# Kernel tuning notes

Measured on AMD Instinct MI355X. Metric: run time of the kernel, lower is better.

The kernel has to match this reference:

```python
import jax, jax.numpy as jnp
import numpy as np

NUM_CODES = 512
DIM = 64
B, M = 32, 64


def setup_inputs() -> dict:
    key = jax.random.key(0)
    k1, k2 = jax.random.split(key)
    inputs = jax.random.normal(k1, (B, M, M, DIM), dtype=jnp.float32)
    # keras 'uniform' initializer is U(-0.05, 0.05)
    embeddings = jax.random.uniform(k2, (NUM_CODES, DIM), dtype=jnp.float32,
                                    minval=-0.05, maxval=0.05)
    return {"inputs": inputs, "embeddings": embeddings}


def reference(inputs, embeddings):
    l2_inputs = jnp.sum(inputs * inputs, axis=-1, keepdims=True)      # [B,M,M,1]
    l2_embeddings = jnp.sum(embeddings * embeddings, axis=-1)          # [K]
    dot = jnp.einsum('bhwd,kd->bhwk', inputs, embeddings)              # [B,M,M,K]
    distance = l2_inputs + l2_embeddings - 2.0 * dot                   # [B,M,M,K]
    codes = jnp.argmin(distance, axis=-1).astype(jnp.int32)            # [B,M,M]
    code_vecs = embeddings[codes]                                      # [B,M,M,D]
    return codes, code_vecs
```

## Files before the change

kernel.cpp:

```cpp
#include <hip/hip_runtime.h>

#define NUM_CODES 512
#define DIM 64
#define NPIX (32 * 64 * 64)
#define CT (NUM_CODES / 16)
#define BLK 256
#define NGRP 2
#define PPB 128

typedef __attribute__((ext_vector_type(8))) short bf16x8;
typedef __attribute__((ext_vector_type(4))) float f32x4;

__device__ __forceinline__ unsigned short f2bf(float f) {
    unsigned u = __float_as_uint(f);
    return (unsigned short)((u + 0x7fffu + ((u >> 16) & 1u)) >> 16);
}
__device__ __forceinline__ float bf2f(unsigned short h) {
    return __uint_as_float(((unsigned)h) << 16);
}

__global__ __launch_bounds__(256) void prep_kernel(
    const float* __restrict__ emb, unsigned short* __restrict__ AH,
    unsigned short* __restrict__ ALO, float* __restrict__ l2e,
    float* __restrict__ l2eh) {
    const int t = blockIdx.x * 256 + threadIdx.x;
    const int e0 = t * 4;
    const int c = e0 >> 6, d0 = e0 & 63;
    const float4 v = *(const float4*)(emb + c * DIM + d0);
    float f[4] = {-v.x, -v.y, -v.z, -v.w};
    unsigned short h[4], l[4];
#pragma unroll
    for (int i = 0; i < 4; ++i) {
        h[i] = f2bf(f[i]);
        l[i] = f2bf(f[i] - bf2f(h[i]));
    }
    const int ct = c >> 4, mr = c & 15, s = d0 >> 5, q = (d0 & 31) >> 3,
              j0 = d0 & 7;
    const int base = ((ct * 2 + s) * 64 + (q * 16 + mr)) * 8 + j0;
    *(ushort4*)(AH + base) = make_ushort4(h[0], h[1], h[2], h[3]);
    *(ushort4*)(ALO + base) = make_ushort4(l[0], l[1], l[2], l[3]);

    if (t < NUM_CODES) {
        const float* e = emb + t * DIM;
        float r[8];
#pragma unroll
        for (int j = 0; j < 8; ++j) {
            float w = e[j];
            r[j] = w * w;
        }
#pragma unroll
        for (int i = 8; i < DIM; i += 8)
#pragma unroll
            for (int j = 0; j < 8; ++j) {
                float w = e[i + j];
                r[j] += w * w;
            }
        float sv =
            ((r[0] + r[1]) + (r[2] + r[3])) + ((r[4] + r[5]) + (r[6] + r[7]));
        l2e[t] = sv;
        l2eh[t] = 0.5f * sv;
    }
}

__global__ __launch_bounds__(BLK, 4) void vq_main(
    const float* __restrict__ x_in, const unsigned short* __restrict__ AH,
    const unsigned short* __restrict__ ALO, const float* __restrict__ l2e,
    const float* __restrict__ l2eh, const float* __restrict__ emb,
    float* __restrict__ codes_out, float* __restrict__ vecs_out) {
    __shared__ float s_l2eh[NUM_CODES];
    __shared__ float s_l2ex[NUM_CODES];
    __shared__ int s_top[PPB][2];
    __shared__ int s_code[PPB];

    const int tid = threadIdx.x, lane = tid & 63, wave = tid >> 6;
    s_l2eh[tid] = l2eh[tid];
    s_l2eh[tid + 256] = l2eh[tid + 256];
    s_l2ex[tid] = l2e[tid];
    s_l2ex[tid + 256] = l2e[tid + 256];
    __syncthreads();

    const int p = lane & 15, q = lane >> 4;
    const int pw = blockIdx.x * PPB + wave * (16 * NGRP);

    bf16x8 bh0[NGRP], bl0[NGRP], bh1[NGRP], bl1[NGRP];
#pragma unroll
    for (int g = 0; g < NGRP; ++g) {
        const float* xb = x_in + (size_t)(pw + g * 16 + p) * DIM + q * 8;
        float4 u0 = *(const float4*)(xb);
        float4 u1 = *(const float4*)(xb + 4);
        float4 u2 = *(const float4*)(xb + 32);
        float4 u3 = *(const float4*)(xb + 36);
        float f0[8] = {u0.x, u0.y, u0.z, u0.w, u1.x, u1.y, u1.z, u1.w};
        float f1[8] = {u2.x, u2.y, u2.z, u2.w, u3.x, u3.y, u3.z, u3.w};
#pragma unroll
        for (int j = 0; j < 8; ++j) {
            unsigned short hh = f2bf(f0[j]);
            bh0[g][j] = (short)hh;
            bl0[g][j] = (short)f2bf(f0[j] - bf2f(hh));
            unsigned short h2 = f2bf(f1[j]);
            bh1[g][j] = (short)h2;
            bl1[g][j] = (short)f2bf(f1[j] - bf2f(h2));
        }
    }

    const int rowbase = q * 4;
    float d1[NGRP], d2[NGRP];
    int k1[NGRP], k2[NGRP];
#pragma unroll
    for (int g = 0; g < NGRP; ++g) {
        d1[g] = 3.4e38f;
        d2[g] = 3.4e38f;
        k1[g] = 0;
        k2[g] = 0;
    }

    const unsigned short* pAH = AH + lane * 8;
    const unsigned short* pAL = ALO + lane * 8;

    bf16x8 a0h = *(const bf16x8*)(pAH);
    bf16x8 a0l = *(const bf16x8*)(pAL);
    bf16x8 a1h = *(const bf16x8*)(pAH + 512);
    bf16x8 a1l = *(const bf16x8*)(pAL + 512);

    for (int ct = 0; ct < CT; ++ct) {
        const int nt = (ct + 1) & (CT - 1);
        const bf16x8 n0h = *(const bf16x8*)(pAH + nt * 1024);
        const bf16x8 n0l = *(const bf16x8*)(pAL + nt * 1024);
        const bf16x8 n1h = *(const bf16x8*)(pAH + nt * 1024 + 512);
        const bf16x8 n1l = *(const bf16x8*)(pAL + nt * 1024 + 512);

        const int kb = ct * 16 + rowbase;
        const f32x4 acc_init = *(const f32x4*)&s_l2eh[kb];

#pragma unroll
        for (int g = 0; g < NGRP; ++g) {
            f32x4 acc = acc_init;
            acc = __builtin_amdgcn_mfma_f32_16x16x32_bf16(a0h, bh0[g], acc, 0, 0, 0);
            acc = __builtin_amdgcn_mfma_f32_16x16x32_bf16(a1h, bh1[g], acc, 0, 0, 0);
            acc = __builtin_amdgcn_mfma_f32_16x16x32_bf16(a0l, bh0[g], acc, 0, 0, 0);
            acc = __builtin_amdgcn_mfma_f32_16x16x32_bf16(a1l, bh1[g], acc, 0, 0, 0);
            acc = __builtin_amdgcn_mfma_f32_16x16x32_bf16(a0h, bl0[g], acc, 0, 0, 0);
            acc = __builtin_amdgcn_mfma_f32_16x16x32_bf16(a1h, bl1[g], acc, 0, 0, 0);

#pragma unroll
            for (int r = 0; r < 4; ++r) {
                const float d = acc[r];
                const int kk = kb + r;
                const bool c = d < d1[g], c2 = d < d2[g];
                const float nd2 = __builtin_amdgcn_fmed3f(d1[g], d2[g], d);
                const int nk2 = c2 ? kk : k2[g];
                k2[g] = c ? k1[g] : nk2;
                k1[g] = c ? kk : k1[g];
                d2[g] = nd2;
                d1[g] = fminf(d1[g], d);
            }
        }
        a0h = n0h;
        a0l = n0l;
        a1h = n1h;
        a1l = n1l;
    }

#pragma unroll
    for (int g = 0; g < NGRP; ++g) {
        float a1 = d1[g], a2 = d2[g];
        int b1 = k1[g], b2 = k2[g];
#pragma unroll
        for (int off = 16; off <= 32; off <<= 1) {
            const float od1 = __shfl_xor(a1, off);
            const int ok1 = __shfl_xor(b1, off);
            const float od2 = __shfl_xor(a2, off);
            const int ok2 = __shfl_xor(b2, off);
            const bool c = od1 < a1;
            const float w1 = c ? od1 : a1;
            const int wk1 = c ? ok1 : b1;
            const float l1 = c ? a1 : od1;
            const int lk1 = c ? b1 : ok1;
            const bool cm = od2 < a2;
            const float m2 = cm ? od2 : a2;
            const int mk2 = cm ? ok2 : b2;
            const bool c3 = m2 < l1;
            a2 = c3 ? m2 : l1;
            b2 = c3 ? mk2 : lk1;
            a1 = w1;
            b1 = wk1;
        }
        if (lane < 16) {
            const int pb = wave * (16 * NGRP) + g * 16 + lane;
            s_top[pb][0] = b1;
            s_top[pb][1] = b2;
        }
    }
    __syncthreads();

    if (tid < PPB) {
        const int pix = blockIdx.x * PPB + tid;
        int ka = s_top[tid][0], kb2 = s_top[tid][1];
        if (kb2 < ka) {
            const int tt = ka;
            ka = kb2;
            kb2 = tt;
        }
        const float* xr = x_in + (size_t)pix * DIM;
        float x[DIM];
#pragma unroll
        for (int jj = 0; jj < 16; ++jj) {
            const float4 v = *(const float4*)(xr + jj * 4);
            x[4 * jj + 0] = v.x;
            x[4 * jj + 1] = v.y;
            x[4 * jj + 2] = v.z;
            x[4 * jj + 3] = v.w;
        }
        float r[8];
#pragma unroll
        for (int j = 0; j < 8; ++j) r[j] = x[j] * x[j];
#pragma unroll
        for (int i = 8; i < DIM; i += 8)
#pragma unroll
            for (int j = 0; j < 8; ++j) r[j] += x[i + j] * x[i + j];
        const float l2x =
            ((r[0] + r[1]) + (r[2] + r[3])) + ((r[4] + r[5]) + (r[6] + r[7]));

        const float* ea = emb + (size_t)ka * DIM;
        float acca = 0.f;
#pragma unroll
        for (int d = 0; d < DIM; ++d) acca = __builtin_fmaf(x[d], ea[d], acca);
        const float da = (l2x + s_l2ex[ka]) - 2.0f * acca;

        const float* eb = emb + (size_t)kb2 * DIM;
        float accb = 0.f;
#pragma unroll
        for (int d = 0; d < DIM; ++d) accb = __builtin_fmaf(x[d], eb[d], accb);
        const float db = (l2x + s_l2ex[kb2]) - 2.0f * accb;

        const int sel = (db < da) ? kb2 : ka;
        s_code[tid] = sel;
        codes_out[pix] = (float)sel;
    }
    __syncthreads();

    const float4* emb4 = (const float4*)emb;
    float4* vout4 = (float4*)(vecs_out + (size_t)blockIdx.x * PPB * DIM);
#pragma unroll
    for (int it = 0; it < (PPB * DIM / 4) / BLK; ++it) {
        const int fidx = tid + it * BLK;
        const int pp = fidx >> 4, dd = fidx & 15;
        vout4[fidx] = emb4[(size_t)s_code[pp] * (DIM / 4) + dd];
    }
}

extern "C" void kernel_launch(void* const* d_in, const int* in_sizes, int n_in,
                              void* d_out, int out_size, void* d_ws,
                              size_t ws_size, hipStream_t stream) {
    const float* x_in = (const float*)d_in[0];
    const float* emb = (const float*)d_in[1];

    unsigned short* AH = (unsigned short*)d_ws;
    unsigned short* ALO = AH + NUM_CODES * DIM;
    float* l2e = (float*)(ALO + NUM_CODES * DIM);
    float* l2eh = l2e + NUM_CODES;

    float* codes_out = (float*)d_out;
    float* vecs_out = (float*)d_out + NPIX;

    hipLaunchKernelGGL(prep_kernel, dim3(32), dim3(256), 0, stream, emb, AH,
                       ALO, l2e, l2eh);
    hipLaunchKernelGGL(vq_main, dim3(NPIX / PPB), dim3(BLK), 0, stream, x_in,
                       AH, ALO, l2e, l2eh, emb, codes_out, vecs_out);
}
```

Measured before the change: 126.2 us.

## Deepen codebook prefetch, split MFMA chains, and parallelize top-2 refinement across all threads

The codebook tile loads are now issued two tiles ahead instead of one, and the loop is unrolled by four to hide global-load latency. Each group's six dependent MFMAs are split into two independent accumulator chains of three and summed afterwards, which shortens the dependency chain. The MFMA block is wrapped in s_setprio. The exact fp32 re-check of the two candidates now runs on all 256 threads, one candidate per thread, with a shuffle to pick the winner, instead of 128 threads each doing two dot products. This costs more registers and each x row is loaded twice.

```diff
diff --git a/kernel.cpp b/kernel.cpp
--- a/kernel.cpp
+++ b/kernel.cpp
@@ -117,34 +117,48 @@
     const unsigned short* pAH = AH + lane * 8;
     const unsigned short* pAL = ALO + lane * 8;
 
-    bf16x8 a0h = *(const bf16x8*)(pAH);
-    bf16x8 a0l = *(const bf16x8*)(pAL);
-    bf16x8 a1h = *(const bf16x8*)(pAH + 512);
-    bf16x8 a1l = *(const bf16x8*)(pAL + 512);
-
+    bf16x8 c0h = *(const bf16x8*)(pAH);
+    bf16x8 c0l = *(const bf16x8*)(pAL);
+    bf16x8 c1h = *(const bf16x8*)(pAH + 512);
+    bf16x8 c1l = *(const bf16x8*)(pAL + 512);
+    bf16x8 p0h = *(const bf16x8*)(pAH + 1024);
+    bf16x8 p0l = *(const bf16x8*)(pAL + 1024);
+    bf16x8 p1h = *(const bf16x8*)(pAH + 1024 + 512);
+    bf16x8 p1l = *(const bf16x8*)(pAL + 1024 + 512);
+
+#pragma unroll 4
     for (int ct = 0; ct < CT; ++ct) {
-        const int nt = (ct + 1) & (CT - 1);
-        const bf16x8 n0h = *(const bf16x8*)(pAH + nt * 1024);
-        const bf16x8 n0l = *(const bf16x8*)(pAL + nt * 1024);
-        const bf16x8 n1h = *(const bf16x8*)(pAH + nt * 1024 + 512);
-        const bf16x8 n1l = *(const bf16x8*)(pAL + nt * 1024 + 512);
+        const int nt = (ct + 2) & (CT - 1);
+        const bf16x8 q0h = *(const bf16x8*)(pAH + nt * 1024);
+        const bf16x8 q0l = *(const bf16x8*)(pAL + nt * 1024);
+        const bf16x8 q1h = *(const bf16x8*)(pAH + nt * 1024 + 512);
+        const bf16x8 q1l = *(const bf16x8*)(pAL + nt * 1024 + 512);
 
         const int kb = ct * 16 + rowbase;
         const f32x4 acc_init = *(const f32x4*)&s_l2eh[kb];
 
+        f32x4 accA[NGRP], accB[NGRP];
+        __builtin_amdgcn_s_setprio(1);
 #pragma unroll
         for (int g = 0; g < NGRP; ++g) {
-            f32x4 acc = acc_init;
-            acc = __builtin_amdgcn_mfma_f32_16x16x32_bf16(a0h, bh0[g], acc, 0, 0, 0);
-            acc = __builtin_amdgcn_mfma_f32_16x16x32_bf16(a1h, bh1[g], acc, 0, 0, 0);
-            acc = __builtin_amdgcn_mfma_f32_16x16x32_bf16(a0l, bh0[g], acc, 0, 0, 0);
-            acc = __builtin_amdgcn_mfma_f32_16x16x32_bf16(a1l, bh1[g], acc, 0, 0, 0);
-            acc = __builtin_amdgcn_mfma_f32_16x16x32_bf16(a0h, bl0[g], acc, 0, 0, 0);
-            acc = __builtin_amdgcn_mfma_f32_16x16x32_bf16(a1h, bl1[g], acc, 0, 0, 0);
-
+            f32x4 a = acc_init;
+            a = __builtin_amdgcn_mfma_f32_16x16x32_bf16(c0h, bh0[g], a, 0, 0, 0);
+            a = __builtin_amdgcn_mfma_f32_16x16x32_bf16(c0l, bh0[g], a, 0, 0, 0);
+            a = __builtin_amdgcn_mfma_f32_16x16x32_bf16(c0h, bl0[g], a, 0, 0, 0);
+            f32x4 b = {0.f, 0.f, 0.f, 0.f};
+            b = __builtin_amdgcn_mfma_f32_16x16x32_bf16(c1h, bh1[g], b, 0, 0, 0);
+            b = __builtin_amdgcn_mfma_f32_16x16x32_bf16(c1l, bh1[g], b, 0, 0, 0);
+            b = __builtin_amdgcn_mfma_f32_16x16x32_bf16(c1h, bl1[g], b, 0, 0, 0);
+            accA[g] = a;
+            accB[g] = b;
+        }
+        __builtin_amdgcn_s_setprio(0);
+
+#pragma unroll
+        for (int g = 0; g < NGRP; ++g) {
 #pragma unroll
             for (int r = 0; r < 4; ++r) {
-                const float d = acc[r];
+                const float d = accA[g][r] + accB[g][r];
                 const int kk = kb + r;
                 const bool c = d < d1[g], c2 = d < d2[g];
                 const float nd2 = __builtin_amdgcn_fmed3f(d1[g], d2[g], d);
@@ -155,10 +169,9 @@
                 d1[g] = fminf(d1[g], d);
             }
         }
-        a0h = n0h;
-        a0l = n0l;
-        a1h = n1h;
-        a1l = n1l;
+
+        c0h = p0h; c0l = p0l; c1h = p1h; c1l = p1l;
+        p0h = q0h; p0l = q0l; p1h = q1h; p1l = q1l;
     }
 
 #pragma unroll
@@ -193,14 +206,10 @@
     }
     __syncthreads();
 
-    if (tid < PPB) {
-        const int pix = blockIdx.x * PPB + tid;
-        int ka = s_top[tid][0], kb2 = s_top[tid][1];
-        if (kb2 < ka) {
-            const int tt = ka;
-            ka = kb2;
-            kb2 = tt;
-        }
+    {
+        const int pixloc = tid >> 1, which = tid & 1;
+        const int pix = blockIdx.x * PPB + pixloc;
+        const int k_me = s_top[pixloc][which];
         const float* xr = x_in + (size_t)pix * DIM;
         float x[DIM];
 #pragma unroll
@@ -221,21 +230,20 @@
         const float l2x =
             ((r[0] + r[1]) + (r[2] + r[3])) + ((r[4] + r[5]) + (r[6] + r[7]));
 
-        const float* ea = emb + (size_t)ka * DIM;
-        float acca = 0.f;
-#pragma unroll
-        for (int d = 0; d < DIM; ++d) acca = __builtin_fmaf(x[d], ea[d], acca);
-        const float da = (l2x + s_l2ex[ka]) - 2.0f * acca;
-
-        const float* eb = emb + (size_t)kb2 * DIM;
-        float accb = 0.f;
-#pragma unroll
-        for (int d = 0; d < DIM; ++d) accb = __builtin_fmaf(x[d], eb[d], accb);
-        const float db = (l2x + s_l2ex[kb2]) - 2.0f * accb;
-
-        const int sel = (db < da) ? kb2 : ka;
-        s_code[tid] = sel;
-        codes_out[pix] = (float)sel;
+        const float* em = emb + (size_t)k_me * DIM;
+        float acc = 0.f;
+#pragma unroll
+        for (int d = 0; d < DIM; ++d) acc = __builtin_fmaf(x[d], em[d], acc);
+        const float d_me = (l2x + s_l2ex[k_me]) - 2.0f * acc;
+
+        const float d_o = __shfl_xor(d_me, 1);
+        const int k_o = __shfl_xor(k_me, 1);
+        const int sel =
+            (d_me < d_o || (d_me == d_o && k_me < k_o)) ? k_me : k_o;
+        if (which == 0) {
+            s_code[pixloc] = sel;
+            codes_out[pix] = (float)sel;
+        }
     }
     __syncthreads();
 
```

Measured after the change: 120.1 us. -4.9%, faster.
